# Kernel tuning notes

Measured on AMD Instinct MI355X. Metric: run time of the kernel, lower is better.

Reference implementation:

```python
import jax, jax.numpy as jnp
import numpy as np

N = 50000      # num nodes
E = 1600000    # num edges (before self-loops)
DIN, DH, DOUT = 256, 128, 64


def _gcn_norm(edge_index, num_nodes):
    # Add self-loops, then symmetric normalization 1/sqrt(deg_i * deg_j)
    loop = jnp.arange(num_nodes, dtype=edge_index.dtype)
    src = jnp.concatenate([edge_index[0], loop])  # [E+N]
    dst = jnp.concatenate([edge_index[1], loop])  # [E+N]
    deg = jax.ops.segment_sum(jnp.ones_like(dst, dtype=jnp.float32), dst,
                              num_segments=num_nodes)
    dinv = jnp.where(deg > 0, jax.lax.rsqrt(deg), 0.0)
    norm = dinv[src] * dinv[dst]  # [E+N]
    return src, dst, norm


def _gcn_conv(x, src, dst, norm, W, b, num_nodes):
    h = x @ W                                  # [N, out] dense transform first
    msg = h[src] * norm[:, None]               # gather + scale  [E+N, out]
    out = jax.ops.segment_sum(msg, dst, num_segments=num_nodes)  # scatter-add
    return out + b


def reference(x, edge_index, W1, b1, W2, b2):
    num_nodes = x.shape[0]
    src, dst, norm = _gcn_norm(edge_index, num_nodes)
    h = _gcn_conv(x, src, dst, norm, W1, b1, num_nodes)
    h = jax.nn.relu(h)
    # dropout(p=0.5) is identity in eval mode
    out = _gcn_conv(h, src, dst, norm, W2, b2, num_nodes)
    return out


def setup_inputs() -> dict:
    key = jax.random.key(0)
    ks = jax.random.split(key, 6)
    x = jax.random.normal(ks[0], (N, DIN), dtype=jnp.float32)
    edge_index = jax.random.randint(ks[1], (2, E), 0, N, dtype=jnp.int32)
    W1 = jax.random.normal(ks[2], (DIN, DH), dtype=jnp.float32) * (1.0 / np.sqrt(DIN))
    b1 = jnp.zeros((DH,), dtype=jnp.float32)
    W2 = jax.random.normal(ks[3], (DH, DOUT), dtype=jnp.float32) * (1.0 / np.sqrt(DH))
    b2 = jnp.zeros((DOUT,), dtype=jnp.float32)
    return {"x": x, "edge_index": edge_index, "W1": W1, "b1": b1, "W2": W2, "b2": b2}
```

## Files before the change

### kernel.cpp

```cpp
#include <hip/hip_runtime.h>

#define DIN 256
#define DH  128
#define DOUT 64
#define BSH  7
#define BNODES 128
#define MAXBUK 400
#define NBLK 512

typedef unsigned int  u32;
typedef unsigned short u16;
typedef __attribute__((ext_vector_type(8))) short bf16x8;
typedef __attribute__((ext_vector_type(4))) float f32x4;

__device__ inline u16 f2bf(float f) {
  u32 u = __float_as_uint(f);
  u32 r = u + 0x7FFF + ((u >> 16) & 1);
  return (u16)(r >> 16);
}
__device__ inline float bf2f_lo(u32 packed) { return __uint_as_float(packed << 16); }
__device__ inline float bf2f_hi(u32 packed) { return __uint_as_float(packed & 0xFFFF0000u); }


__global__ __launch_bounds__(256) void hist_kernel(const int* __restrict__ dst,
    int* __restrict__ counts, int E, int nbuk) {
  __shared__ int h[MAXBUK];
  int tid = threadIdx.x, b = blockIdx.x;
  for (int i = tid; i < nbuk; i += 256) h[i] = 0;
  __syncthreads();
  int ech = (E + NBLK - 1) / NBLK;
  int e0 = b * ech, e1 = min(E, e0 + ech);
  for (int e = e0 + tid; e < e1; e += 256)
    atomicAdd(&h[dst[e] >> BSH], 1);
  __syncthreads();
  for (int i = tid; i < nbuk; i += 256) counts[(size_t)i * NBLK + b] = h[i];
}

__global__ __launch_bounds__(256) void col_scan(int* __restrict__ counts,
    int* __restrict__ colsum, int nbuk) {
  __shared__ int sm[256];
  __shared__ int carry;
  int buk = blockIdx.x, t = threadIdx.x;
  if (t == 0) carry = 0;
  __syncthreads();
  int* row = counts + (size_t)buk * NBLK;
  for (int base = 0; base < NBLK; base += 256) {
    int v = row[base + t];
    sm[t] = v;
    __syncthreads();
    for (int d = 1; d < 256; d <<= 1) {
      int a = (t >= d) ? sm[t - d] : 0;
      __syncthreads();
      sm[t] += a;
      __syncthreads();
    }
    int excl = sm[t] - v + carry;
    row[base + t] = excl;
    __syncthreads();
    if (t == 255) carry = excl + v;
    __syncthreads();
  }
  if (t == 0) colsum[buk] = carry;
}

__global__ __launch_bounds__(256) void scan_block(int* partial, int* total_out, int nb, int n) {
  __shared__ int sm[256];
  __shared__ int carry;
  int t = threadIdx.x;
  if (t == 0) carry = 0;
  __syncthreads();
  for (int base = 0; base < nb; base += 256) {
    int g = base + t;
    int v = (g < nb) ? partial[g] : 0;
    sm[t] = v;
    __syncthreads();
    for (int d = 1; d < 256; d <<= 1) {
      int add = (t >= d) ? sm[t - d] : 0;
      __syncthreads();
      sm[t] += add;
      __syncthreads();
    }
    int excl = sm[t] - v + carry;
    if (g < nb) partial[g] = excl;
    __syncthreads();
    if (t == 255) carry = excl + v;
    __syncthreads();
  }
  if (t == 0) total_out[n] = carry;
}

__global__ __launch_bounds__(256) void scatter_kernel(const int* __restrict__ src,
    const int* __restrict__ dst, const int* __restrict__ counts,
    const int* __restrict__ bb, u32* __restrict__ ebuf, int E, int nbuk) {
  __shared__ int cur[MAXBUK];
  int tid = threadIdx.x, b = blockIdx.x;
  for (int i = tid; i < nbuk; i += 256)
    cur[i] = bb[i] + counts[(size_t)i * NBLK + b];
  __syncthreads();
  int ech = (E + NBLK - 1) / NBLK;
  int e0 = b * ech, e1 = min(E, e0 + ech);
  for (int e = e0 + tid; e < e1; e += 256) {
    int d = dst[e];
    int r = atomicAdd(&cur[d >> BSH], 1);
    ebuf[r] = (u32)src[e] | ((u32)(d & (BNODES - 1)) << 16);
  }
}

__global__ __launch_bounds__(256) void bucket_node_count(const u32* __restrict__ ebuf,
    const int* __restrict__ bb, int* __restrict__ cnt, int N) {
  __shared__ int c[BNODES];
  int b = blockIdx.x, tid = threadIdx.x;
  if (tid < BNODES) c[tid] = 0;
  __syncthreads();
  int e0 = bb[b], e1 = bb[b + 1];
  for (int e = e0 + tid; e < e1; e += 256)
    atomicAdd(&c[ebuf[e] >> 16], 1);
  __syncthreads();
  int node = b * BNODES + tid;
  if (tid < BNODES && node < N) cnt[node] = c[tid];
}

__global__ __launch_bounds__(256) void reduce_chunks(const int* __restrict__ cnt,
                                                     int* __restrict__ partial, int n) {
  int t = threadIdx.x;
  int g = blockIdx.x * 256 + t;
  int v = (g < n) ? cnt[g] : 0;
  #pragma unroll
  for (int o = 32; o > 0; o >>= 1) v += __shfl_down(v, o, 64);
  __shared__ int sm[4];
  if ((t & 63) == 0) sm[t >> 6] = v;
  __syncthreads();
  if (t == 0) partial[blockIdx.x] = sm[0] + sm[1] + sm[2] + sm[3];
}

__global__ __launch_bounds__(256) void scan_chunks(const int* __restrict__ cnt,
    const int* __restrict__ chunkoff, int* __restrict__ rowptr,
    float* __restrict__ dinv, int n) {
  __shared__ int sm[256];
  int t = threadIdx.x, g = blockIdx.x * 256 + t;
  int v = (g < n) ? cnt[g] : 0;
  sm[t] = v;
  __syncthreads();
  for (int d = 1; d < 256; d <<= 1) {
    int add = (t >= d) ? sm[t - d] : 0;
    __syncthreads();
    sm[t] += add;
    __syncthreads();
  }
  if (g < n) {
    rowptr[g] = sm[t] - v + chunkoff[blockIdx.x];
    dinv[g] = rsqrtf((float)(v + 1));
  }
}

__global__ __launch_bounds__(256) void bucket_fill(const u32* __restrict__ ebuf,
    const int* __restrict__ bb, const int* __restrict__ rowptr, int* __restrict__ csr) {
  __shared__ int c[BNODES];
  int b = blockIdx.x, tid = threadIdx.x;
  if (tid < BNODES) c[tid] = 0;
  __syncthreads();
  int e0 = bb[b], e1 = bb[b + 1];
  for (int e = e0 + tid; e < e1; e += 256) {
    u32 p = ebuf[e];
    int nl = p >> 16;
    int r = atomicAdd(&c[nl], 1);
    csr[rowptr[b * BNODES + nl] + r] = (int)(p & 0xFFFFu);
  }
}


__global__ __launch_bounds__(256) void w_prep(const float* __restrict__ W1,
    const float* __restrict__ W2, u16* __restrict__ w1t, u16* __restrict__ w2t) {
  int t = blockIdx.x * 256 + threadIdx.x;
  if (t < DH * DIN) {
    int n = t >> 8, k = t & 255;
    w1t[t] = f2bf(W1[k * DH + n]);
  } else {
    int t2 = t - DH * DIN;
    int n = t2 >> 7, k = t2 & 127;
    w2t[t2] = f2bf(W2[k * DOUT + n]);
  }
}


__global__ __launch_bounds__(256) void gemm1_mfma(const float* __restrict__ x,
    const u16* __restrict__ w1t, const float* __restrict__ dinv,
    u16* __restrict__ h1, int M) {
  __shared__ u16 As[64][72];
  __shared__ u16 Bs[128][72];
  const int tid = threadIdx.x;
  const int lane = tid & 63, w = tid >> 6;
  const int row16 = lane & 15, quad = lane >> 4;
  const int rowBase = blockIdx.x * 64;
  f32x4 acc[8];
  #pragma unroll
  for (int nt = 0; nt < 8; ++nt) acc[nt] = (f32x4)(0.f);

  for (int kt = 0; kt < DIN; kt += 64) {
    {
      int r = tid >> 2, kq = tid & 3;
      int grow = rowBase + r;
      #pragma unroll
      for (int i = 0; i < 4; ++i) {
        float4 v = make_float4(0.f, 0.f, 0.f, 0.f);
        if (grow < M) v = *(const float4*)&x[(size_t)grow * DIN + kt + kq * 16 + i * 4];
        u32 lo = (u32)f2bf(v.x) | ((u32)f2bf(v.y) << 16);
        u32 hi = (u32)f2bf(v.z) | ((u32)f2bf(v.w) << 16);
        *(uint2*)&As[r][kq * 16 + i * 4] = make_uint2(lo, hi);
      }
    }
    {
      int n = tid >> 1, half = tid & 1;
      const uint4* s = (const uint4*)&w1t[n * DIN + kt + half * 32];
      uint4* d = (uint4*)&Bs[n][half * 32];
      d[0] = s[0]; d[1] = s[1]; d[2] = s[2]; d[3] = s[3];
    }
    __syncthreads();
    #pragma unroll
    for (int ks = 0; ks < 64; ks += 32) {
      bf16x8 a = *(bf16x8*)&As[w * 16 + row16][ks + quad * 8];
      #pragma unroll
      for (int nt = 0; nt < 8; ++nt) {
        bf16x8 b = *(bf16x8*)&Bs[nt * 16 + row16][ks + quad * 8];
        acc[nt] = __builtin_amdgcn_mfma_f32_16x16x32_bf16(a, b, acc[nt], 0, 0, 0);
      }
    }
    __syncthreads();
  }
  #pragma unroll
  for (int reg = 0; reg < 4; ++reg) {
    int row = rowBase + w * 16 + quad * 4 + reg;
    if (row < M) {
      float s = dinv[row];
      #pragma unroll
      for (int nt = 0; nt < 8; ++nt)
        h1[(size_t)row * DH + nt * 16 + row16] = f2bf(acc[nt][reg] * s);
    }
  }
}


__global__ __launch_bounds__(256) void gemm2_mfma(const u16* __restrict__ g1,
    const u16* __restrict__ w2t, const float* __restrict__ dinv,
    u16* __restrict__ h2, int M) {
  __shared__ u16 As[64][136];
  __shared__ u16 Bs[64][136];
  const int tid = threadIdx.x;
  const int lane = tid & 63, w = tid >> 6;
  const int row16 = lane & 15, quad = lane >> 4;
  const int rowBase = blockIdx.x * 64;
  f32x4 acc[4];
  #pragma unroll
  for (int nt = 0; nt < 4; ++nt) acc[nt] = (f32x4)(0.f);

  #pragma unroll
  for (int i = 0; i < 4; ++i) {
    int flat = i * 256 + tid;
    int r = flat >> 4, c = flat & 15;
    int grow = rowBase + r;
    uint4 v = make_uint4(0, 0, 0, 0);
    if (grow < M) v = *(const uint4*)&g1[(size_t)grow * DH + c * 8];
    *(uint4*)&As[r][c * 8] = v;
  }
  #pragma unroll
  for (int i = 0; i < 4; ++i) {
    int flat = i * 256 + tid;
    int r = flat >> 4, c = flat & 15;
    *(uint4*)&Bs[r][c * 8] = *(const uint4*)&w2t[r * DH + c * 8];
  }
  __syncthreads();
  #pragma unroll
  for (int ks = 0; ks < 128; ks += 32) {
    bf16x8 a = *(bf16x8*)&As[w * 16 + row16][ks + quad * 8];
    #pragma unroll
    for (int nt = 0; nt < 4; ++nt) {
      bf16x8 b = *(bf16x8*)&Bs[nt * 16 + row16][ks + quad * 8];
      acc[nt] = __builtin_amdgcn_mfma_f32_16x16x32_bf16(a, b, acc[nt], 0, 0, 0);
    }
  }
  #pragma unroll
  for (int reg = 0; reg < 4; ++reg) {
    int row = rowBase + w * 16 + quad * 4 + reg;
    if (row < M) {
      float s = dinv[row];
      #pragma unroll
      for (int nt = 0; nt < 4; ++nt)
        h2[(size_t)row * DOUT + nt * 16 + row16] = f2bf(acc[nt][reg] * s);
    }
  }
}


__global__ __launch_bounds__(256) void aggregate1(const u16* __restrict__ h,
    const int* __restrict__ rowptr, const int* __restrict__ csr,
    const float* __restrict__ dinv, const float* __restrict__ bias,
    u16* __restrict__ out, int n) {
  const int lane = threadIdx.x & 63;
  const int sub = lane >> 4;
  const int l16 = lane & 15;
  int node = blockIdx.x * 4 + (threadIdx.x >> 6);
  if (node >= n) return;
  node = __builtin_amdgcn_readfirstlane(node);
  const float di = dinv[node];

  float a[8];
  {
    uint4 v = *(const uint4*)&h[(size_t)node * DH + l16 * 8];
    float ms = (sub == 0) ? 1.f : 0.f;
    a[0] = ms * bf2f_lo(v.x); a[1] = ms * bf2f_hi(v.x);
    a[2] = ms * bf2f_lo(v.y); a[3] = ms * bf2f_hi(v.y);
    a[4] = ms * bf2f_lo(v.z); a[5] = ms * bf2f_hi(v.z);
    a[6] = ms * bf2f_lo(v.w); a[7] = ms * bf2f_hi(v.w);
  }

  int p = rowptr[node];
  const int pe = rowptr[node + 1];
  while (p < pe) {
    int g = p + lane;
    int si = (g < pe) ? csr[g] : 0;
    int rem = pe - p; if (rem > 64) rem = 64;
    int t = 0;
    for (; t + 16 <= rem; t += 16) {
      #pragma unroll
      for (int q = 0; q < 4; ++q) {
        int idx = __shfl(si, t + q * 4 + sub, 64);
        uint4 v = *(const uint4*)&h[(size_t)idx * DH + l16 * 8];
        a[0] += bf2f_lo(v.x); a[1] += bf2f_hi(v.x);
        a[2] += bf2f_lo(v.y); a[3] += bf2f_hi(v.y);
        a[4] += bf2f_lo(v.z); a[5] += bf2f_hi(v.z);
        a[6] += bf2f_lo(v.w); a[7] += bf2f_hi(v.w);
      }
    }
    for (; t < rem; t += 4) {
      int e = t + sub;
      int idx = __shfl(si, e & 63, 64);
      uint4 v = *(const uint4*)&h[(size_t)idx * DH + l16 * 8];
      float m = (e < rem) ? 1.f : 0.f;
      a[0] = fmaf(m, bf2f_lo(v.x), a[0]); a[1] = fmaf(m, bf2f_hi(v.x), a[1]);
      a[2] = fmaf(m, bf2f_lo(v.y), a[2]); a[3] = fmaf(m, bf2f_hi(v.y), a[3]);
      a[4] = fmaf(m, bf2f_lo(v.z), a[4]); a[5] = fmaf(m, bf2f_hi(v.z), a[5]);
      a[6] = fmaf(m, bf2f_lo(v.w), a[6]); a[7] = fmaf(m, bf2f_hi(v.w), a[7]);
    }
    p += 64;
  }

  #pragma unroll
  for (int i = 0; i < 8; ++i) {
    a[i] += __shfl_xor(a[i], 16, 64);
    a[i] += __shfl_xor(a[i], 32, 64);
  }

  if (sub == 0) {
    const int c0 = l16 * 8;
    float4 b0 = *(const float4*)&bias[c0];
    float4 b1 = *(const float4*)&bias[c0 + 4];
    float r0 = fmaxf(fmaf(a[0], di, b0.x), 0.f);
    float r1 = fmaxf(fmaf(a[1], di, b0.y), 0.f);
    float r2 = fmaxf(fmaf(a[2], di, b0.z), 0.f);
    float r3 = fmaxf(fmaf(a[3], di, b0.w), 0.f);
    float r4 = fmaxf(fmaf(a[4], di, b1.x), 0.f);
    float r5 = fmaxf(fmaf(a[5], di, b1.y), 0.f);
    float r6 = fmaxf(fmaf(a[6], di, b1.z), 0.f);
    float r7 = fmaxf(fmaf(a[7], di, b1.w), 0.f);
    u32 pk[4];
    pk[0] = (u32)f2bf(r0) | ((u32)f2bf(r1) << 16);
    pk[1] = (u32)f2bf(r2) | ((u32)f2bf(r3) << 16);
    pk[2] = (u32)f2bf(r4) | ((u32)f2bf(r5) << 16);
    pk[3] = (u32)f2bf(r6) | ((u32)f2bf(r7) << 16);
    *(uint4*)&out[(size_t)node * DH + c0] = *(uint4*)pk;
  }
}

__global__ __launch_bounds__(256) void aggregate2(const u16* __restrict__ h,
    const int* __restrict__ rowptr, const int* __restrict__ csr,
    const float* __restrict__ dinv, const float* __restrict__ bias,
    float* __restrict__ out, int n) {
  const int lane = threadIdx.x & 63;
  const int sub = lane >> 3;
  const int l8 = lane & 7;
  int node = blockIdx.x * 4 + (threadIdx.x >> 6);
  if (node >= n) return;
  node = __builtin_amdgcn_readfirstlane(node);
  const float di = dinv[node];

  float a[8];
  {
    uint4 v = *(const uint4*)&h[(size_t)node * DOUT + l8 * 8];
    float ms = (sub == 0) ? 1.f : 0.f;
    a[0] = ms * bf2f_lo(v.x); a[1] = ms * bf2f_hi(v.x);
    a[2] = ms * bf2f_lo(v.y); a[3] = ms * bf2f_hi(v.y);
    a[4] = ms * bf2f_lo(v.z); a[5] = ms * bf2f_hi(v.z);
    a[6] = ms * bf2f_lo(v.w); a[7] = ms * bf2f_hi(v.w);
  }

  int p = rowptr[node];
  const int pe = rowptr[node + 1];
  while (p < pe) {
    int g = p + lane;
    int si = (g < pe) ? csr[g] : 0;
    int rem = pe - p; if (rem > 64) rem = 64;
    int t = 0;
    for (; t + 32 <= rem; t += 32) {
      #pragma unroll
      for (int q = 0; q < 4; ++q) {
        int idx = __shfl(si, t + q * 8 + sub, 64);
        uint4 v = *(const uint4*)&h[(size_t)idx * DOUT + l8 * 8];
        a[0] += bf2f_lo(v.x); a[1] += bf2f_hi(v.x);
        a[2] += bf2f_lo(v.y); a[3] += bf2f_hi(v.y);
        a[4] += bf2f_lo(v.z); a[5] += bf2f_hi(v.z);
        a[6] += bf2f_lo(v.w); a[7] += bf2f_hi(v.w);
      }
    }
    for (; t < rem; t += 8) {
      int e = t + sub;
      int idx = __shfl(si, e & 63, 64);
      uint4 v = *(const uint4*)&h[(size_t)idx * DOUT + l8 * 8];
      float m = (e < rem) ? 1.f : 0.f;
      a[0] = fmaf(m, bf2f_lo(v.x), a[0]); a[1] = fmaf(m, bf2f_hi(v.x), a[1]);
      a[2] = fmaf(m, bf2f_lo(v.y), a[2]); a[3] = fmaf(m, bf2f_hi(v.y), a[3]);
      a[4] = fmaf(m, bf2f_lo(v.z), a[4]); a[5] = fmaf(m, bf2f_hi(v.z), a[5]);
      a[6] = fmaf(m, bf2f_lo(v.w), a[6]); a[7] = fmaf(m, bf2f_hi(v.w), a[7]);
    }
    p += 64;
  }

  #pragma unroll
  for (int i = 0; i < 8; ++i) {
    a[i] += __shfl_xor(a[i], 8, 64);
    a[i] += __shfl_xor(a[i], 16, 64);
    a[i] += __shfl_xor(a[i], 32, 64);
  }

  if (sub == 0) {
    const int c0 = l8 * 8;
    float4 b0 = *(const float4*)&bias[c0];
    float4 b1 = *(const float4*)&bias[c0 + 4];
    float4 r0, r1;
    r0.x = fmaf(a[0], di, b0.x);
    r0.y = fmaf(a[1], di, b0.y);
    r0.z = fmaf(a[2], di, b0.z);
    r0.w = fmaf(a[3], di, b0.w);
    r1.x = fmaf(a[4], di, b1.x);
    r1.y = fmaf(a[5], di, b1.y);
    r1.z = fmaf(a[6], di, b1.z);
    r1.w = fmaf(a[7], di, b1.w);
    *(float4*)&out[(size_t)node * DOUT + c0] = r0;
    *(float4*)&out[(size_t)node * DOUT + c0 + 4] = r1;
  }
}


extern "C" void kernel_launch(void* const* d_in, const int* in_sizes, int n_in,
                              void* d_out, int out_size, void* d_ws, size_t ws_size,
                              hipStream_t stream) {
  const float* x  = (const float*)d_in[0];
  const int*   ei = (const int*)d_in[1];
  const float* W1 = (const float*)d_in[2];
  const float* b1 = (const float*)d_in[3];
  const float* W2 = (const float*)d_in[4];
  const float* b2 = (const float*)d_in[5];
  float* out = (float*)d_out;

  const int N = in_sizes[0] / DIN;
  const int E = in_sizes[1] / 2;
  const int* src = ei;
  const int* dst = ei + E;
  const int NB = (N + 255) / 256;
  const int nbuk = (N + BNODES - 1) / BNODES;

  char* ws = (char*)d_ws;
  size_t o = 0;
  auto alloc = [&](size_t bytes) { size_t r = o; o += (bytes + 511) & ~(size_t)511; return r; };
  size_t colsum_o  = alloc((size_t)(nbuk + 1) * 4);
  size_t counts_o  = alloc((size_t)nbuk * NBLK * 4);
  size_t rowptr_o  = alloc((size_t)(N + 1) * 4);
  size_t partial_o = alloc((size_t)NB * 4);
  size_t dinv_o    = alloc((size_t)N * 4);
  size_t cnt_o     = alloc((size_t)N * 4);
  size_t w1t_o     = alloc((size_t)DH * DIN * 2);
  size_t w2t_o     = alloc((size_t)DOUT * DH * 2);
  size_t csr_o     = alloc((size_t)E * 4);
  size_t h1_o      = alloc((size_t)N * DH * 2);
  size_t g1_o      = alloc((size_t)N * DH * 2);
  size_t h2_o      = h1_o;
  size_t ebuf_o    = g1_o;

  int*   colsum  = (int*)(ws + colsum_o);
  int*   counts  = (int*)(ws + counts_o);
  int*   rowptr  = (int*)(ws + rowptr_o);
  int*   partial = (int*)(ws + partial_o);
  float* dinv    = (float*)(ws + dinv_o);
  int*   cnt     = (int*)(ws + cnt_o);
  u16*   w1t     = (u16*)(ws + w1t_o);
  u16*   w2t     = (u16*)(ws + w2t_o);
  int*   csr     = (int*)(ws + csr_o);
  u16*   h1      = (u16*)(ws + h1_o);
  u16*   g1      = (u16*)(ws + g1_o);
  u16*   h2      = (u16*)(ws + h2_o);
  u32*   ebuf    = (u32*)(ws + ebuf_o);

  w_prep<<<(DH * DIN + DOUT * DH) / 256, 256, 0, stream>>>(W1, W2, w1t, w2t);
  hist_kernel<<<NBLK, 256, 0, stream>>>(dst, counts, E, nbuk);
  col_scan<<<nbuk, 256, 0, stream>>>(counts, colsum, nbuk);
  scan_block<<<1, 256, 0, stream>>>(colsum, colsum, nbuk, nbuk);
  scatter_kernel<<<NBLK, 256, 0, stream>>>(src, dst, counts, colsum, ebuf, E, nbuk);
  bucket_node_count<<<nbuk, 256, 0, stream>>>(ebuf, colsum, cnt, N);
  reduce_chunks<<<NB, 256, 0, stream>>>(cnt, partial, N);
  scan_block<<<1, 256, 0, stream>>>(partial, rowptr, NB, N);
  scan_chunks<<<NB, 256, 0, stream>>>(cnt, partial, rowptr, dinv, N);
  bucket_fill<<<nbuk, 256, 0, stream>>>(ebuf, colsum, rowptr, csr);

  gemm1_mfma<<<(N + 63) / 64, 256, 0, stream>>>(x, w1t, dinv, h1, N);
  aggregate1<<<(N + 3) / 4, 256, 0, stream>>>(h1, rowptr, csr, dinv, b1, g1, N);
  gemm2_mfma<<<(N + 63) / 64, 256, 0, stream>>>(g1, w2t, dinv, h2, N);
  aggregate2<<<(N + 3) / 4, 256, 0, stream>>>(h2, rowptr, csr, dinv, b2, out, N);
}
```

Baseline: 244.2 us.

## Batch gathers, prefetch CSR indices, and map two nodes per wave in aggregate2

```diff
diff --git a/kernel.cpp b/kernel.cpp
--- a/kernel.cpp
+++ b/kernel.cpp
@@ -302,10 +302,11 @@
   if (node >= n) return;
   node = __builtin_amdgcn_readfirstlane(node);
   const float di = dinv[node];
+  const size_t coff = (size_t)l16 * 8;
 
   float a[8];
   {
-    uint4 v = *(const uint4*)&h[(size_t)node * DH + l16 * 8];
+    uint4 v = *(const uint4*)&h[(size_t)node * DH + coff];
     float ms = (sub == 0) ? 1.f : 0.f;
     a[0] = ms * bf2f_lo(v.x); a[1] = ms * bf2f_hi(v.x);
     a[2] = ms * bf2f_lo(v.y); a[3] = ms * bf2f_hi(v.y);
@@ -315,33 +316,47 @@
 
   int p = rowptr[node];
   const int pe = rowptr[node + 1];
+  int g = p + lane;
+  int si = (g < pe) ? csr[g] : 0;
   while (p < pe) {
-    int g = p + lane;
-    int si = (g < pe) ? csr[g] : 0;
     int rem = pe - p; if (rem > 64) rem = 64;
+    int gn = p + 64 + lane;
+    int si_next = (gn < pe) ? csr[gn] : 0;
     int t = 0;
-    for (; t + 16 <= rem; t += 16) {
+    for (; t + 32 <= rem; t += 32) {
+      uint4 v[8];
+      #pragma unroll
+      for (int q = 0; q < 8; ++q) {
+        int idx = __shfl(si, t + q * 4 + sub, 64);
+        v[q] = *(const uint4*)&h[(size_t)idx * DH + coff];
+      }
+      #pragma unroll
+      for (int q = 0; q < 8; ++q) {
+        a[0] += bf2f_lo(v[q].x); a[1] += bf2f_hi(v[q].x);
+        a[2] += bf2f_lo(v[q].y); a[3] += bf2f_hi(v[q].y);
+        a[4] += bf2f_lo(v[q].z); a[5] += bf2f_hi(v[q].z);
+        a[6] += bf2f_lo(v[q].w); a[7] += bf2f_hi(v[q].w);
+      }
+    }
+    for (; t < rem; t += 16) {
+      uint4 v[4]; float m[4];
       #pragma unroll
       for (int q = 0; q < 4; ++q) {
-        int idx = __shfl(si, t + q * 4 + sub, 64);
-        uint4 v = *(const uint4*)&h[(size_t)idx * DH + l16 * 8];
-        a[0] += bf2f_lo(v.x); a[1] += bf2f_hi(v.x);
-        a[2] += bf2f_lo(v.y); a[3] += bf2f_hi(v.y);
-        a[4] += bf2f_lo(v.z); a[5] += bf2f_hi(v.z);
-        a[6] += bf2f_lo(v.w); a[7] += bf2f_hi(v.w);
-      }
-    }
-    for (; t < rem; t += 4) {
-      int e = t + sub;
-      int idx = __shfl(si, e & 63, 64);
-      uint4 v = *(const uint4*)&h[(size_t)idx * DH + l16 * 8];
-      float m = (e < rem) ? 1.f : 0.f;
-      a[0] = fmaf(m, bf2f_lo(v.x), a[0]); a[1] = fmaf(m, bf2f_hi(v.x), a[1]);
-      a[2] = fmaf(m, bf2f_lo(v.y), a[2]); a[3] = fmaf(m, bf2f_hi(v.y), a[3]);
-      a[4] = fmaf(m, bf2f_lo(v.z), a[4]); a[5] = fmaf(m, bf2f_hi(v.z), a[5]);
-      a[6] = fmaf(m, bf2f_lo(v.w), a[6]); a[7] = fmaf(m, bf2f_hi(v.w), a[7]);
+        int e = t + q * 4 + sub;
+        int idx = __shfl(si, e, 64);
+        v[q] = *(const uint4*)&h[(size_t)idx * DH + coff];
+        m[q] = (e < rem) ? 1.f : 0.f;
+      }
+      #pragma unroll
+      for (int q = 0; q < 4; ++q) {
+        a[0] = fmaf(m[q], bf2f_lo(v[q].x), a[0]); a[1] = fmaf(m[q], bf2f_hi(v[q].x), a[1]);
+        a[2] = fmaf(m[q], bf2f_lo(v[q].y), a[2]); a[3] = fmaf(m[q], bf2f_hi(v[q].y), a[3]);
+        a[4] = fmaf(m[q], bf2f_lo(v[q].z), a[4]); a[5] = fmaf(m[q], bf2f_hi(v[q].z), a[5]);
+        a[6] = fmaf(m[q], bf2f_lo(v[q].w), a[6]); a[7] = fmaf(m[q], bf2f_hi(v[q].w), a[7]);
+      }
     }
     p += 64;
+    si = si_next;
   }
 
   #pragma unroll
@@ -376,16 +391,17 @@
     const float* __restrict__ dinv, const float* __restrict__ bias,
     float* __restrict__ out, int n) {
   const int lane = threadIdx.x & 63;
-  const int sub = lane >> 3;
+  const int halfbase = lane & 32;
+  const int sub = (lane >> 3) & 3;
   const int l8 = lane & 7;
-  int node = blockIdx.x * 4 + (threadIdx.x >> 6);
+  const int node = blockIdx.x * 8 + ((threadIdx.x >> 6) << 1) + (halfbase >> 5);
   if (node >= n) return;
-  node = __builtin_amdgcn_readfirstlane(node);
   const float di = dinv[node];
+  const size_t coff = (size_t)l8 * 8;
 
   float a[8];
   {
-    uint4 v = *(const uint4*)&h[(size_t)node * DOUT + l8 * 8];
+    uint4 v = *(const uint4*)&h[(size_t)node * DOUT + coff];
     float ms = (sub == 0) ? 1.f : 0.f;
     a[0] = ms * bf2f_lo(v.x); a[1] = ms * bf2f_hi(v.x);
     a[2] = ms * bf2f_lo(v.y); a[3] = ms * bf2f_hi(v.y);
@@ -395,40 +411,53 @@
 
   int p = rowptr[node];
   const int pe = rowptr[node + 1];
+  int g = p + (lane & 31);
+  int si = (g < pe) ? csr[g] : 0;
   while (p < pe) {
-    int g = p + lane;
-    int si = (g < pe) ? csr[g] : 0;
-    int rem = pe - p; if (rem > 64) rem = 64;
+    int rem = pe - p; if (rem > 32) rem = 32;
+    int gn = p + 32 + (lane & 31);
+    int si_next = (gn < pe) ? csr[gn] : 0;
     int t = 0;
     for (; t + 32 <= rem; t += 32) {
+      uint4 v[8];
+      #pragma unroll
+      for (int q = 0; q < 8; ++q) {
+        int idx = __shfl(si, halfbase | (q * 4 + sub), 64);
+        v[q] = *(const uint4*)&h[(size_t)idx * DOUT + coff];
+      }
+      #pragma unroll
+      for (int q = 0; q < 8; ++q) {
+        a[0] += bf2f_lo(v[q].x); a[1] += bf2f_hi(v[q].x);
+        a[2] += bf2f_lo(v[q].y); a[3] += bf2f_hi(v[q].y);
+        a[4] += bf2f_lo(v[q].z); a[5] += bf2f_hi(v[q].z);
+        a[6] += bf2f_lo(v[q].w); a[7] += bf2f_hi(v[q].w);
+      }
+    }
+    for (; t < rem; t += 16) {
+      uint4 v[4]; float m[4];
       #pragma unroll
       for (int q = 0; q < 4; ++q) {
-        int idx = __shfl(si, t + q * 8 + sub, 64);
-        uint4 v = *(const uint4*)&h[(size_t)idx * DOUT + l8 * 8];
-        a[0] += bf2f_lo(v.x); a[1] += bf2f_hi(v.x);
-        a[2] += bf2f_lo(v.y); a[3] += bf2f_hi(v.y);
-        a[4] += bf2f_lo(v.z); a[5] += bf2f_hi(v.z);
-        a[6] += bf2f_lo(v.w); a[7] += bf2f_hi(v.w);
-      }
-    }
-    for (; t < rem; t += 8) {
-      int e = t + sub;
-      int idx = __shfl(si, e & 63, 64);
-      uint4 v = *(const uint4*)&h[(size_t)idx * DOUT + l8 * 8];
-      float m = (e < rem) ? 1.f : 0.f;
-      a[0] = fmaf(m, bf2f_lo(v.x), a[0]); a[1] = fmaf(m, bf2f_hi(v.x), a[1]);
-      a[2] = fmaf(m, bf2f_lo(v.y), a[2]); a[3] = fmaf(m, bf2f_hi(v.y), a[3]);
-      a[4] = fmaf(m, bf2f_lo(v.z), a[4]); a[5] = fmaf(m, bf2f_hi(v.z), a[5]);
-      a[6] = fmaf(m, bf2f_lo(v.w), a[6]); a[7] = fmaf(m, bf2f_hi(v.w), a[7]);
-    }
-    p += 64;
+        int e = t + q * 4 + sub;
+        int idx = __shfl(si, halfbase | e, 64);
+        v[q] = *(const uint4*)&h[(size_t)idx * DOUT + coff];
+        m[q] = (e < rem) ? 1.f : 0.f;
+      }
+      #pragma unroll
+      for (int q = 0; q < 4; ++q) {
+        a[0] = fmaf(m[q], bf2f_lo(v[q].x), a[0]); a[1] = fmaf(m[q], bf2f_hi(v[q].x), a[1]);
+        a[2] = fmaf(m[q], bf2f_lo(v[q].y), a[2]); a[3] = fmaf(m[q], bf2f_hi(v[q].y), a[3]);
+        a[4] = fmaf(m[q], bf2f_lo(v[q].z), a[4]); a[5] = fmaf(m[q], bf2f_hi(v[q].z), a[5]);
+        a[6] = fmaf(m[q], bf2f_lo(v[q].w), a[6]); a[7] = fmaf(m[q], bf2f_hi(v[q].w), a[7]);
+      }
+    }
+    p += 32;
+    si = si_next;
   }
 
   #pragma unroll
   for (int i = 0; i < 8; ++i) {
     a[i] += __shfl_xor(a[i], 8, 64);
     a[i] += __shfl_xor(a[i], 16, 64);
-    a[i] += __shfl_xor(a[i], 32, 64);
   }
 
   if (sub == 0) {
@@ -513,5 +542,5 @@
   gemm1_mfma<<<(N + 63) / 64, 256, 0, stream>>>(x, w1t, dinv, h1, N);
   aggregate1<<<(N + 3) / 4, 256, 0, stream>>>(h1, rowptr, csr, dinv, b1, g1, N);
   gemm2_mfma<<<(N + 63) / 64, 256, 0, stream>>>(g1, w2t, dinv, h2, N);
-  aggregate2<<<(N + 3) / 4, 256, 0, stream>>>(h2, rowptr, csr, dinv, b2, out, N);
-}
+  aggregate2<<<(N + 7) / 8, 256, 0, stream>>>(h2, rowptr, csr, dinv, b2, out, N);
+}
```

New measurement: 247.3 us. No clear change (+1.3%).

## Fuse second GEMM into first aggregation and shrink CSR indices to 16-bit

Applied to the files above, without the earlier changes.

```diff
diff --git a/kernel.cpp b/kernel.cpp
--- a/kernel.cpp
+++ b/kernel.cpp
@@ -107,7 +107,7 @@
 }
 
 __global__ __launch_bounds__(256) void bucket_node_count(const u32* __restrict__ ebuf,
-    const int* __restrict__ bb, int* __restrict__ cnt, int N) {
+    const int* __restrict__ bb, int* __restrict__ cnt, int* __restrict__ bpartial, int N) {
   __shared__ int c[BNODES];
   int b = blockIdx.x, tid = threadIdx.x;
   if (tid < BNODES) c[tid] = 0;
@@ -118,19 +118,12 @@
   __syncthreads();
   int node = b * BNODES + tid;
   if (tid < BNODES && node < N) cnt[node] = c[tid];
-}
-
-__global__ __launch_bounds__(256) void reduce_chunks(const int* __restrict__ cnt,
-                                                     int* __restrict__ partial, int n) {
-  int t = threadIdx.x;
-  int g = blockIdx.x * 256 + t;
-  int v = (g < n) ? cnt[g] : 0;
-  #pragma unroll
-  for (int o = 32; o > 0; o >>= 1) v += __shfl_down(v, o, 64);
-  __shared__ int sm[4];
-  if ((t & 63) == 0) sm[t >> 6] = v;
-  __syncthreads();
-  if (t == 0) partial[blockIdx.x] = sm[0] + sm[1] + sm[2] + sm[3];
+  if (tid < 64) {
+    int s = c[tid] + c[tid + 64];
+    #pragma unroll
+    for (int o = 32; o > 0; o >>= 1) s += __shfl_down(s, o, 64);
+    if (tid == 0) bpartial[b] = s;
+  }
 }
 
 __global__ __launch_bounds__(256) void scan_chunks(const int* __restrict__ cnt,
@@ -148,13 +141,13 @@
     __syncthreads();
   }
   if (g < n) {
-    rowptr[g] = sm[t] - v + chunkoff[blockIdx.x];
+    rowptr[g] = sm[t] - v + chunkoff[blockIdx.x * 2];
     dinv[g] = rsqrtf((float)(v + 1));
   }
 }
 
 __global__ __launch_bounds__(256) void bucket_fill(const u32* __restrict__ ebuf,
-    const int* __restrict__ bb, const int* __restrict__ rowptr, int* __restrict__ csr) {
+    const int* __restrict__ bb, const int* __restrict__ rowptr, u16* __restrict__ csr) {
   __shared__ int c[BNODES];
   int b = blockIdx.x, tid = threadIdx.x;
   if (tid < BNODES) c[tid] = 0;
@@ -164,21 +157,23 @@
     u32 p = ebuf[e];
     int nl = p >> 16;
     int r = atomicAdd(&c[nl], 1);
-    csr[rowptr[b * BNODES + nl] + r] = (int)(p & 0xFFFFu);
+    csr[rowptr[b * BNODES + nl] + r] = (u16)(p & 0xFFFFu);
   }
 }
 
 
 __global__ __launch_bounds__(256) void w_prep(const float* __restrict__ W1,
-    const float* __restrict__ W2, u16* __restrict__ w1t, u16* __restrict__ w2t) {
+    const float* __restrict__ W2, u16* __restrict__ w1t, u32* __restrict__ w2p) {
   int t = blockIdx.x * 256 + threadIdx.x;
   if (t < DH * DIN) {
     int n = t >> 8, k = t & 255;
     w1t[t] = f2bf(W1[k * DH + n]);
   } else {
     int t2 = t - DH * DIN;
-    int n = t2 >> 7, k = t2 & 127;
-    w2t[t2] = f2bf(W2[k * DOUT + n]);
+    int kk = t2 >> 6, j = t2 & 63;
+    u32 lo = f2bf(W2[(2 * kk) * DOUT + j]);
+    u32 hi = f2bf(W2[(2 * kk + 1) * DOUT + j]);
+    w2p[t2] = lo | (hi << 16);
   }
 }
 
@@ -240,72 +235,34 @@
 }
 
 
-__global__ __launch_bounds__(256) void gemm2_mfma(const u16* __restrict__ g1,
-    const u16* __restrict__ w2t, const float* __restrict__ dinv,
-    u16* __restrict__ h2, int M) {
-  __shared__ u16 As[64][136];
-  __shared__ u16 Bs[64][136];
+__global__ __launch_bounds__(256) void aggregate1_fused(const u16* __restrict__ h,
+    const int* __restrict__ rowptr, const u16* __restrict__ csr,
+    const float* __restrict__ dinv, const float* __restrict__ bias,
+    const u32* __restrict__ w2p, u16* __restrict__ h2, int n) {
+  __shared__ u32 w2s[64 * 64];
+  __shared__ float rowbuf[4][128];
   const int tid = threadIdx.x;
-  const int lane = tid & 63, w = tid >> 6;
-  const int row16 = lane & 15, quad = lane >> 4;
-  const int rowBase = blockIdx.x * 64;
-  f32x4 acc[4];
-  #pragma unroll
-  for (int nt = 0; nt < 4; ++nt) acc[nt] = (f32x4)(0.f);
-
-  #pragma unroll
-  for (int i = 0; i < 4; ++i) {
-    int flat = i * 256 + tid;
-    int r = flat >> 4, c = flat & 15;
-    int grow = rowBase + r;
-    uint4 v = make_uint4(0, 0, 0, 0);
-    if (grow < M) v = *(const uint4*)&g1[(size_t)grow * DH + c * 8];
-    *(uint4*)&As[r][c * 8] = v;
-  }
-  #pragma unroll
-  for (int i = 0; i < 4; ++i) {
-    int flat = i * 256 + tid;
-    int r = flat >> 4, c = flat & 15;
-    *(uint4*)&Bs[r][c * 8] = *(const uint4*)&w2t[r * DH + c * 8];
-  }
-  __syncthreads();
-  #pragma unroll
-  for (int ks = 0; ks < 128; ks += 32) {
-    bf16x8 a = *(bf16x8*)&As[w * 16 + row16][ks + quad * 8];
+  {
+    const uint4* s = (const uint4*)w2p;
+    uint4* d = (uint4*)w2s;
     #pragma unroll
-    for (int nt = 0; nt < 4; ++nt) {
-      bf16x8 b = *(bf16x8*)&Bs[nt * 16 + row16][ks + quad * 8];
-      acc[nt] = __builtin_amdgcn_mfma_f32_16x16x32_bf16(a, b, acc[nt], 0, 0, 0);
-    }
-  }
-  #pragma unroll
-  for (int reg = 0; reg < 4; ++reg) {
-    int row = rowBase + w * 16 + quad * 4 + reg;
-    if (row < M) {
-      float s = dinv[row];
-      #pragma unroll
-      for (int nt = 0; nt < 4; ++nt)
-        h2[(size_t)row * DOUT + nt * 16 + row16] = f2bf(acc[nt][reg] * s);
-    }
-  }
-}
-
-
-__global__ __launch_bounds__(256) void aggregate1(const u16* __restrict__ h,
-    const int* __restrict__ rowptr, const int* __restrict__ csr,
-    const float* __restrict__ dinv, const float* __restrict__ bias,
-    u16* __restrict__ out, int n) {
-  const int lane = threadIdx.x & 63;
+    for (int i = 0; i < 4; ++i) d[i * 256 + tid] = s[i * 256 + tid];
+  }
+  __syncthreads();
+
+  const int lane = tid & 63;
+  const int wv = tid >> 6;
   const int sub = lane >> 4;
   const int l16 = lane & 15;
-  int node = blockIdx.x * 4 + (threadIdx.x >> 6);
+  int node = blockIdx.x * 4 + wv;
   if (node >= n) return;
   node = __builtin_amdgcn_readfirstlane(node);
   const float di = dinv[node];
+  const size_t coff = (size_t)l16 * 8;
 
   float a[8];
   {
-    uint4 v = *(const uint4*)&h[(size_t)node * DH + l16 * 8];
+    uint4 v = *(const uint4*)&h[(size_t)node * DH + coff];
     float ms = (sub == 0) ? 1.f : 0.f;
     a[0] = ms * bf2f_lo(v.x); a[1] = ms * bf2f_hi(v.x);
     a[2] = ms * bf2f_lo(v.y); a[3] = ms * bf2f_hi(v.y);
@@ -317,14 +274,14 @@
   const int pe = rowptr[node + 1];
   while (p < pe) {
     int g = p + lane;
-    int si = (g < pe) ? csr[g] : 0;
+    int si = (g < pe) ? (int)csr[g] : 0;
     int rem = pe - p; if (rem > 64) rem = 64;
     int t = 0;
     for (; t + 16 <= rem; t += 16) {
       #pragma unroll
       for (int q = 0; q < 4; ++q) {
         int idx = __shfl(si, t + q * 4 + sub, 64);
-        uint4 v = *(const uint4*)&h[(size_t)idx * DH + l16 * 8];
+        uint4 v = *(const uint4*)&h[(size_t)idx * DH + coff];
         a[0] += bf2f_lo(v.x); a[1] += bf2f_hi(v.x);
         a[2] += bf2f_lo(v.y); a[3] += bf2f_hi(v.y);
         a[4] += bf2f_lo(v.z); a[5] += bf2f_hi(v.z);
@@ -334,7 +291,7 @@
     for (; t < rem; t += 4) {
       int e = t + sub;
       int idx = __shfl(si, e & 63, 64);
-      uint4 v = *(const uint4*)&h[(size_t)idx * DH + l16 * 8];
+      uint4 v = *(const uint4*)&h[(size_t)idx * DH + coff];
       float m = (e < rem) ? 1.f : 0.f;
       a[0] = fmaf(m, bf2f_lo(v.x), a[0]); a[1] = fmaf(m, bf2f_hi(v.x), a[1]);
       a[2] = fmaf(m, bf2f_lo(v.y), a[2]); a[3] = fmaf(m, bf2f_hi(v.y), a[3]);
@@ -350,29 +307,48 @@
     a[i] += __shfl_xor(a[i], 32, 64);
   }
 
+  const int c0 = l16 * 8;
+  float4 b0 = *(const float4*)&bias[c0];
+  float4 b1v = *(const float4*)&bias[c0 + 4];
+  float f0 = fmaxf(fmaf(a[0], di, b0.x), 0.f);
+  float f1 = fmaxf(fmaf(a[1], di, b0.y), 0.f);
+  float f2 = fmaxf(fmaf(a[2], di, b0.z), 0.f);
+  float f3 = fmaxf(fmaf(a[3], di, b0.w), 0.f);
+  float f4 = fmaxf(fmaf(a[4], di, b1v.x), 0.f);
+  float f5 = fmaxf(fmaf(a[5], di, b1v.y), 0.f);
+  float f6 = fmaxf(fmaf(a[6], di, b1v.z), 0.f);
+  float f7 = fmaxf(fmaf(a[7], di, b1v.w), 0.f);
   if (sub == 0) {
-    const int c0 = l16 * 8;
-    float4 b0 = *(const float4*)&bias[c0];
-    float4 b1 = *(const float4*)&bias[c0 + 4];
-    float r0 = fmaxf(fmaf(a[0], di, b0.x), 0.f);
-    float r1 = fmaxf(fmaf(a[1], di, b0.y), 0.f);
-    float r2 = fmaxf(fmaf(a[2], di, b0.z), 0.f);
-    float r3 = fmaxf(fmaf(a[3], di, b0.w), 0.f);
-    float r4 = fmaxf(fmaf(a[4], di, b1.x), 0.f);
-    float r5 = fmaxf(fmaf(a[5], di, b1.y), 0.f);
-    float r6 = fmaxf(fmaf(a[6], di, b1.z), 0.f);
-    float r7 = fmaxf(fmaf(a[7], di, b1.w), 0.f);
-    u32 pk[4];
-    pk[0] = (u32)f2bf(r0) | ((u32)f2bf(r1) << 16);
-    pk[1] = (u32)f2bf(r2) | ((u32)f2bf(r3) << 16);
-    pk[2] = (u32)f2bf(r4) | ((u32)f2bf(r5) << 16);
-    pk[3] = (u32)f2bf(r6) | ((u32)f2bf(r7) << 16);
-    *(uint4*)&out[(size_t)node * DH + c0] = *(uint4*)pk;
-  }
-}
+    float* rb = &rowbuf[wv][c0];
+    rb[0] = f0; rb[1] = f1; rb[2] = f2; rb[3] = f3;
+    rb[4] = f4; rb[5] = f5; rb[6] = f6; rb[7] = f7;
+  }
+  asm volatile("s_waitcnt lgkmcnt(0)" ::: "memory");
+  __builtin_amdgcn_sched_barrier(0);
+
+  const float* rb = rowbuf[wv];
+  const u32* wrow = &w2s[lane];
+  float o = 0.f;
+  #pragma unroll
+  for (int kk = 0; kk < 64; kk += 4) {
+    float4 r01 = *(const float4*)&rb[2 * kk];
+    float4 r23 = *(const float4*)&rb[2 * kk + 4];
+    u32 w0 = wrow[(kk + 0) * 64];
+    u32 w1 = wrow[(kk + 1) * 64];
+    u32 w2v = wrow[(kk + 2) * 64];
+    u32 w3 = wrow[(kk + 3) * 64];
+    o = fmaf(r01.x, bf2f_lo(w0), o); o = fmaf(r01.y, bf2f_hi(w0), o);
+    o = fmaf(r01.z, bf2f_lo(w1), o); o = fmaf(r01.w, bf2f_hi(w1), o);
+    o = fmaf(r23.x, bf2f_lo(w2v), o); o = fmaf(r23.y, bf2f_hi(w2v), o);
+    o = fmaf(r23.z, bf2f_lo(w3), o); o = fmaf(r23.w, bf2f_hi(w3), o);
+  }
+  o *= di;
+  h2[(size_t)node * DOUT + lane] = f2bf(o);
+}
+
 
 __global__ __launch_bounds__(256) void aggregate2(const u16* __restrict__ h,
-    const int* __restrict__ rowptr, const int* __restrict__ csr,
+    const int* __restrict__ rowptr, const u16* __restrict__ csr,
     const float* __restrict__ dinv, const float* __restrict__ bias,
     float* __restrict__ out, int n) {
   const int lane = threadIdx.x & 63;
@@ -382,10 +358,11 @@
   if (node >= n) return;
   node = __builtin_amdgcn_readfirstlane(node);
   const float di = dinv[node];
+  const size_t coff = (size_t)l8 * 8;
 
   float a[8];
   {
-    uint4 v = *(const uint4*)&h[(size_t)node * DOUT + l8 * 8];
+    uint4 v = *(const uint4*)&h[(size_t)node * DOUT + coff];
     float ms = (sub == 0) ? 1.f : 0.f;
     a[0] = ms * bf2f_lo(v.x); a[1] = ms * bf2f_hi(v.x);
     a[2] = ms * bf2f_lo(v.y); a[3] = ms * bf2f_hi(v.y);
@@ -397,14 +374,14 @@
   const int pe = rowptr[node + 1];
   while (p < pe) {
     int g = p + lane;
-    int si = (g < pe) ? csr[g] : 0;
+    int si = (g < pe) ? (int)csr[g] : 0;
     int rem = pe - p; if (rem > 64) rem = 64;
     int t = 0;
     for (; t + 32 <= rem; t += 32) {
       #pragma unroll
       for (int q = 0; q < 4; ++q) {
         int idx = __shfl(si, t + q * 8 + sub, 64);
-        uint4 v = *(const uint4*)&h[(size_t)idx * DOUT + l8 * 8];
+        uint4 v = *(const uint4*)&h[(size_t)idx * DOUT + coff];
         a[0] += bf2f_lo(v.x); a[1] += bf2f_hi(v.x);
         a[2] += bf2f_lo(v.y); a[3] += bf2f_hi(v.y);
         a[4] += bf2f_lo(v.z); a[5] += bf2f_hi(v.z);
@@ -414,7 +391,7 @@
     for (; t < rem; t += 8) {
       int e = t + sub;
       int idx = __shfl(si, e & 63, 64);
-      uint4 v = *(const uint4*)&h[(size_t)idx * DOUT + l8 * 8];
+      uint4 v = *(const uint4*)&h[(size_t)idx * DOUT + coff];
       float m = (e < rem) ? 1.f : 0.f;
       a[0] = fmaf(m, bf2f_lo(v.x), a[0]); a[1] = fmaf(m, bf2f_hi(v.x), a[1]);
       a[2] = fmaf(m, bf2f_lo(v.y), a[2]); a[3] = fmaf(m, bf2f_hi(v.y), a[3]);
@@ -474,16 +451,15 @@
   size_t colsum_o  = alloc((size_t)(nbuk + 1) * 4);
   size_t counts_o  = alloc((size_t)nbuk * NBLK * 4);
   size_t rowptr_o  = alloc((size_t)(N + 1) * 4);
-  size_t partial_o = alloc((size_t)NB * 4);
+  size_t partial_o = alloc((size_t)(nbuk + 1) * 4);
   size_t dinv_o    = alloc((size_t)N * 4);
   size_t cnt_o     = alloc((size_t)N * 4);
   size_t w1t_o     = alloc((size_t)DH * DIN * 2);
-  size_t w2t_o     = alloc((size_t)DOUT * DH * 2);
-  size_t csr_o     = alloc((size_t)E * 4);
+  size_t w2p_o     = alloc((size_t)(DH / 2) * DOUT * 4);
+  size_t csr_o     = alloc((size_t)E * 2);
   size_t h1_o      = alloc((size_t)N * DH * 2);
-  size_t g1_o      = alloc((size_t)N * DH * 2);
-  size_t h2_o      = h1_o;
-  size_t ebuf_o    = g1_o;
+  size_t big_o     = alloc((size_t)E * 4);
+  size_t h2_o      = big_o;
 
   int*   colsum  = (int*)(ws + colsum_o);
   int*   counts  = (int*)(ws + counts_o);
@@ -492,26 +468,23 @@
   float* dinv    = (float*)(ws + dinv_o);
   int*   cnt     = (int*)(ws + cnt_o);
   u16*   w1t     = (u16*)(ws + w1t_o);
-  u16*   w2t     = (u16*)(ws + w2t_o);
-  int*   csr     = (int*)(ws + csr_o);
+  u32*   w2p     = (u32*)(ws + w2p_o);
+  u16*   csr     = (u16*)(ws + csr_o);
   u16*   h1      = (u16*)(ws + h1_o);
-  u16*   g1      = (u16*)(ws + g1_o);
+  u32*   ebuf    = (u32*)(ws + big_o);
   u16*   h2      = (u16*)(ws + h2_o);
-  u32*   ebuf    = (u32*)(ws + ebuf_o);
-
-  w_prep<<<(DH * DIN + DOUT * DH) / 256, 256, 0, stream>>>(W1, W2, w1t, w2t);
+
+  w_prep<<<(DH * DIN + (DH / 2) * DOUT) / 256, 256, 0, stream>>>(W1, W2, w1t, w2p);
   hist_kernel<<<NBLK, 256, 0, stream>>>(dst, counts, E, nbuk);
   col_scan<<<nbuk, 256, 0, stream>>>(counts, colsum, nbuk);
   scan_block<<<1, 256, 0, stream>>>(colsum, colsum, nbuk, nbuk);
   scatter_kernel<<<NBLK, 256, 0, stream>>>(src, dst, counts, colsum, ebuf, E, nbuk);
-  bucket_node_count<<<nbuk, 256, 0, stream>>>(ebuf, colsum, cnt, N);
-  reduce_chunks<<<NB, 256, 0, stream>>>(cnt, partial, N);
-  scan_block<<<1, 256, 0, stream>>>(partial, rowptr, NB, N);
+  bucket_node_count<<<nbuk, 256, 0, stream>>>(ebuf, colsum, cnt, partial, N);
+  scan_block<<<1, 256, 0, stream>>>(partial, rowptr, nbuk, N);
   scan_chunks<<<NB, 256, 0, stream>>>(cnt, partial, rowptr, dinv, N);
   bucket_fill<<<nbuk, 256, 0, stream>>>(ebuf, colsum, rowptr, csr);
 
   gemm1_mfma<<<(N + 63) / 64, 256, 0, stream>>>(x, w1t, dinv, h1, N);
-  aggregate1<<<(N + 3) / 4, 256, 0, stream>>>(h1, rowptr, csr, dinv, b1, g1, N);
-  gemm2_mfma<<<(N + 63) / 64, 256, 0, stream>>>(g1, w2t, dinv, h2, N);
+  aggregate1_fused<<<(N + 3) / 4, 256, 0, stream>>>(h1, rowptr, csr, dinv, b1, w2p, h2, N);
   aggregate2<<<(N + 3) / 4, 256, 0, stream>>>(h2, rowptr, csr, dinv, b2, out, N);
 }
```

Result: no change. 241.7 us (-1.0%).
